# Kernel optimization log

Hardware: AMD Instinct MI355X
Metric: run time of the kernel (lower is better)

Reference implementation:

```python
import jax, jax.numpy as jnp
import numpy as np

B, P, ENC, DEC, ATT, EMB, V, MEM, TCAP = 64, 196, 2048, 512, 512, 512, 10000, 128, 22
T = TCAP - 1  # max decode length (caption_lengths - 1)


def setup_inputs() -> dict:
    key = jax.random.key(0)
    ks = iter(jax.random.split(key, 32))
    def w(shape, s=0.02):
        return (jax.random.normal(next(ks), shape, jnp.float32) * s)
    encoder_out = jax.random.normal(next(ks), (B, P, ENC), jnp.float32)
    encoded_captions = jax.random.randint(next(ks), (B, TCAP), 0, V)
    lens = np.sort(np.asarray(jax.random.randint(next(ks), (B,), 5, TCAP + 1)))[::-1].copy()
    lens[0] = TCAP  # ensure max(decode_lengths) == T
    caption_lengths = jnp.asarray(lens, jnp.int32)
    return {
        'encoder_out': encoder_out,
        'encoded_captions': encoded_captions,
        'caption_lengths': caption_lengths,
        'emb_table': w((V, EMB), 0.05),
        # Linear weights stored as [in, out] (torch W.T), so y = x @ W + b
        'W_enc': w((ENC, ATT)), 'b_enc': jnp.zeros((ATT,), jnp.float32),
        'W_dec': w((DEC, ATT)), 'b_dec': jnp.zeros((ATT,), jnp.float32),
        'W_full': w((ATT, 1)), 'b_full': jnp.zeros((1,), jnp.float32),
        'W_inith': w((ENC, DEC)), 'b_inith': jnp.zeros((DEC,), jnp.float32),
        'W_initc': w((ENC, DEC)), 'b_initc': jnp.zeros((DEC,), jnp.float32),
        'W_beta': w((DEC, ENC)), 'b_beta': jnp.zeros((ENC,), jnp.float32),
        # LSTMCell (torch gate order i, f, g, o), stored as [in, 4*dec]
        'W_ih': w((EMB + ENC, 4 * DEC)), 'b_ih': jnp.zeros((4 * DEC,), jnp.float32),
        'W_hh': w((DEC, 4 * DEC)), 'b_hh': jnp.zeros((4 * DEC,), jnp.float32),
        'memory_bank': jax.random.normal(next(ks), (MEM, DEC), jnp.float32),
        'W_fc': w((DEC, V)), 'b_fc': jnp.zeros((V,), jnp.float32),
    }


def _decode(encoder_out, encoded_captions, caption_lengths, emb_table,
            W_enc, b_enc, W_dec, b_dec, W_full, b_full,
            W_inith, b_inith, W_initc, b_initc, W_beta, b_beta,
            W_ih, b_ih, W_hh, b_hh, memory_bank, W_fc, b_fc):
    dec_len = caption_lengths - 1  # decode_lengths
    embs = emb_table[encoded_captions]                 # [B, TCAP, EMB]
    mean_enc = encoder_out.mean(axis=1)                # [B, ENC]
    h0 = mean_enc @ W_inith + b_inith
    c0 = mean_enc @ W_initc + b_initc
    att1 = encoder_out @ W_enc + b_enc                 # [B, P, ATT] precomputed

    x_seq = jnp.swapaxes(embs[:, :T, :], 0, 1)         # [T, B, EMB]
    mask_seq = jnp.arange(T)[:, None] < dec_len[None, :]  # [T, B]

    def step(carry, inp):
        h, c = carry
        x_t, m = inp                                   # [B,EMB], [B]
        # attention
        att2 = h @ W_dec + b_dec                       # [B, ATT]
        e = (jax.nn.relu(att1 + att2[:, None, :]) @ W_full)[..., 0] + b_full[0]  # [B, P]
        alpha = jax.nn.softmax(e, axis=1)
        awe = jnp.einsum('bpe,bp->be', encoder_out, alpha)  # [B, ENC]
        gate = jax.nn.sigmoid(h @ W_beta + b_beta)
        awe = gate * awe
        # LSTMCell
        xi = jnp.concatenate([x_t, awe], axis=1)
        gates = xi @ W_ih + b_ih + h @ W_hh + b_hh      # [B, 4*DEC]
        gi, gf, gg, go = jnp.split(gates, 4, axis=1)
        c_new = jax.nn.sigmoid(gf) * c + jax.nn.sigmoid(gi) * jnp.tanh(gg)
        h_new = jax.nn.sigmoid(go) * jnp.tanh(c_new)
        # hash memory
        sim = h_new @ memory_bank.T                    # [B, MEM]
        h_new = h_new + jax.nn.softmax(sim, axis=1) @ memory_bank
        # fc (dropout = identity in eval)
        preds = h_new @ W_fc + b_fc                    # [B, V]
        m2 = m[:, None]
        h = jnp.where(m2, h_new, h)
        c = jnp.where(m2, c_new, c)
        preds = jnp.where(m2, preds, 0.0)
        alpha = jnp.where(m2, alpha, 0.0)
        return (h, c), (preds, alpha)

    (_, _), (preds_seq, alpha_seq) = jax.lax.scan(step, (h0, c0), (x_seq, mask_seq))
    predictions = jnp.swapaxes(preds_seq, 0, 1)        # [B, T, V]
    alphas = jnp.swapaxes(alpha_seq, 0, 1)             # [B, T, P]
    return predictions, dec_len, alphas


def reference(encoder_out, encoded_captions, caption_lengths, emb_table,
              W_enc, b_enc, W_dec, b_dec, W_full, b_full,
              W_inith, b_inith, W_initc, b_initc, W_beta, b_beta,
              W_ih, b_ih, W_hh, b_hh, memory_bank, W_fc, b_fc):
    return _decode(encoder_out, encoded_captions, caption_lengths, emb_table,
                   W_enc, b_enc, W_dec, b_dec, W_full, b_full,
                   W_inith, b_inith, W_initc, b_initc, W_beta, b_beta,
                   W_ih, b_ih, W_hh, b_hh, memory_bank, W_fc, b_fc)
```

## Files before the change

kernel.cpp:

```cpp
#include <hip/hip_runtime.h>

#define BB   64
#define PP   196
#define ENCD 2048
#define DECD 512
#define VV   10000
#define TT   21
#define KIH  2560

typedef __attribute__((ext_vector_type(8))) short bf16x8;
typedef __attribute__((ext_vector_type(4))) float f32x4;

__device__ __forceinline__ float sigm(float x)   { return 1.f / (1.f + __expf(-x)); }
__device__ __forceinline__ float tanh_f(float x) { return 1.f - 2.f / (1.f + __expf(2.f * x)); }
__device__ __forceinline__ ushort f2bf(float x) {
    unsigned u = __float_as_uint(x);
    unsigned r = (u + 0x7FFFu + ((u >> 16) & 1u)) >> 16;
    return (ushort)r;
}
__device__ __forceinline__ float bf2f(short u) {
    return __uint_as_float(((unsigned)(ushort)u) << 16);
}
union U8 { float4 f4; ushort u[8]; };


__global__ void k_cvt(const float* __restrict__ in, ushort* __restrict__ out, int n4) {
    int i = blockIdx.x * 256 + threadIdx.x;
    if (i >= n4) return;
    float4 v = ((const float4*)in)[i];
    ushort4 o; o.x = f2bf(v.x); o.y = f2bf(v.y); o.z = f2bf(v.z); o.w = f2bf(v.w);
    ((ushort4*)out)[i] = o;
}

__global__ void k_mean16(const ushort* __restrict__ encB, float* __restrict__ mean) {
    int idx = blockIdx.x * 256 + threadIdx.x;
    int b = idx >> 10, e2 = idx & 1023;
    const uint* p = (const uint*)encB + (size_t)b * PP * 1024 + e2;
    float s0 = 0.f, s1 = 0.f;
    #pragma unroll 7
    for (int i = 0; i < PP; ++i) {
        uint v = p[(size_t)i * 1024];
        s0 += __uint_as_float(v << 16);
        s1 += __uint_as_float(v & 0xffff0000u);
    }
    mean[b * 2048 + e2 * 2]     = s0 * (1.f / 196.f);
    mean[b * 2048 + e2 * 2 + 1] = s1 * (1.f / 196.f);
}

__global__ __launch_bounds__(256) void k_ipart(const float* __restrict__ mean,
        const float* __restrict__ Wh, const float* __restrict__ Wc,
        float* __restrict__ ipart) {
    __shared__ alignas(16) float As[32][68];
    __shared__ alignas(16) float Bs[32][68];
    const int n0 = blockIdx.x * 64;
    const int kc = blockIdx.y;
    const int mat = blockIdx.z;
    const float* Bp = mat ? Wc : Wh;
    const int tid = threadIdx.x, tx = tid & 15, ty = tid >> 4;
    float acc[4][4] = {};
    for (int k0 = 0; k0 < 512; k0 += 32) {
        #pragma unroll
        for (int p = 0; p < 2; ++p) {
            int c = p * 256 + tid;
            int m = c >> 3, k4 = (c & 7) * 4;
            float4 v = *(const float4*)(mean + m * 2048 + kc * 512 + k0 + k4);
            As[k4 + 0][m] = v.x; As[k4 + 1][m] = v.y; As[k4 + 2][m] = v.z; As[k4 + 3][m] = v.w;
            int kb = c >> 4, n4 = (c & 15) * 4;
            float4 w = *(const float4*)(Bp + (size_t)(kc * 512 + k0 + kb) * 512 + n0 + n4);
            *(float4*)&Bs[kb][n4] = w;
        }
        __syncthreads();
        #pragma unroll 8
        for (int k = 0; k < 32; ++k) {
            float4 a = *(const float4*)&As[k][ty * 4];
            float4 b = *(const float4*)&Bs[k][tx * 4];
            float av[4] = {a.x, a.y, a.z, a.w}, bv[4] = {b.x, b.y, b.z, b.w};
            #pragma unroll
            for (int i = 0; i < 4; ++i)
                #pragma unroll
                for (int j = 0; j < 4; ++j) acc[i][j] += av[i] * bv[j];
        }
        __syncthreads();
    }
    #pragma unroll
    for (int i = 0; i < 4; ++i) {
        int m = ty * 4 + i;
        #pragma unroll
        for (int j = 0; j < 4; ++j) {
            int n = n0 + tx * 4 + j;
            ipart[((size_t)(mat * 4 + kc) * BB + m) * 512 + n] = acc[i][j];
        }
    }
}

__global__ void k_ifin(const float* __restrict__ ipart,
                       const float* __restrict__ bh, const float* __restrict__ bc,
                       float* __restrict__ h, float* __restrict__ c, ushort* __restrict__ hB) {
    int idx = blockIdx.x * 256 + threadIdx.x;
    int mat = idx >> 15, rem = idx & 32767;
    int b = rem >> 9, d = rem & 511;
    float s = 0.f;
    #pragma unroll
    for (int kc = 0; kc < 4; ++kc) s += ipart[((size_t)(mat * 4 + kc) * BB + b) * 512 + d];
    if (mat) c[rem] = s + bc[d];
    else { float v = s + bh[d]; h[rem] = v; hB[rem] = f2bf(v); }
}

__global__ __launch_bounds__(256) void k_tcvt_all(
        const float* __restrict__ Wenc, const float* __restrict__ Wdec,
        const float* __restrict__ Wbeta, const float* __restrict__ Whh,
        const float* __restrict__ Wih, const float* __restrict__ Wfc,
        ushort* __restrict__ WencT, ushort* __restrict__ WdecT,
        ushort* __restrict__ WbetaT, ushort* __restrict__ WhhT,
        ushort* __restrict__ WihT, ushort* __restrict__ WfcT) {
    __shared__ float lds[64 * 65];
    int l = blockIdx.x;
    const float* in; ushort* out; int K, N, KT;
    if (l < 256)       { in = Wenc;  out = WencT;  K = 2048; N = 512;   KT = 32; }
    else if (l < 320)  { l -= 256;  in = Wdec;  out = WdecT;  K = 512;  N = 512;   KT = 8; }
    else if (l < 576)  { l -= 320;  in = Wbeta; out = WbetaT; K = 512;  N = 2048;  KT = 8; }
    else if (l < 832)  { l -= 576;  in = Whh;   out = WhhT;   K = 512;  N = 2048;  KT = 8; }
    else if (l < 2112) { l -= 832;  in = Wih;   out = WihT;   K = KIH;  N = 2048;  KT = 40; }
    else               { l -= 2112; in = Wfc;   out = WfcT;   K = 512;  N = 10000; KT = 8; }
    const int k0 = (l % KT) * 64, n0 = (l / KT) * 64;
    const int tid = threadIdx.x;
    for (int i = tid; i < 4096; i += 256) {
        int kk = i >> 6, nn = i & 63;
        float v = 0.f;
        if (n0 + nn < N) v = in[(size_t)(k0 + kk) * N + n0 + nn];
        lds[nn * 65 + kk] = v;
    }
    __syncthreads();
    for (int i = tid; i < 4096; i += 256) {
        int nn = i >> 6, kk = i & 63;
        out[(size_t)(n0 + nn) * K + k0 + kk] = f2bf(lds[nn * 65 + kk]);
    }
}

__global__ __launch_bounds__(256) void k_att1_256(const ushort* __restrict__ A,
        const ushort* __restrict__ Bt, const float* __restrict__ bias,
        ushort* __restrict__ C) {
    __shared__ alignas(16) ushort As[64 * 64];
    __shared__ alignas(16) ushort Bs[256 * 64];
    const int n0 = blockIdx.x * 256;
    const int m0 = blockIdx.y * 64;
    const int tid = threadIdx.x, wid = tid >> 6, lane = tid & 63;
    f32x4 acc[4][4] = {};
    for (int k0 = 0; k0 < 2048; k0 += 64) {
        #pragma unroll
        for (int p = 0; p < 2; ++p) {
            int c = p * 256 + tid;
            int r = c >> 3, cc = c & 7;
            float4 v = *(const float4*)(A + (size_t)(m0 + r) * 2048 + k0 + cc * 8);
            *(float4*)(As + r * 64 + ((cc ^ (r & 7)) * 8)) = v;
        }
        #pragma unroll
        for (int p = 0; p < 8; ++p) {
            int c = p * 256 + tid;
            int r = c >> 3, cc = c & 7;
            float4 v = *(const float4*)(Bt + (size_t)(n0 + r) * 2048 + k0 + cc * 8);
            *(float4*)(Bs + r * 64 + ((cc ^ (r & 7)) * 8)) = v;
        }
        __syncthreads();
        #pragma unroll
        for (int kk = 0; kk < 2; ++kk) {
            int ci = kk * 4 + (lane >> 4);
            bf16x8 afrag[4], bfrag[4];
            #pragma unroll
            for (int m = 0; m < 4; ++m) {
                int row = m * 16 + (lane & 15);
                afrag[m] = *(const bf16x8*)(As + row * 64 + ((ci ^ (row & 7)) * 8));
            }
            #pragma unroll
            for (int n = 0; n < 4; ++n) {
                int col = wid * 64 + n * 16 + (lane & 15);
                bfrag[n] = *(const bf16x8*)(Bs + col * 64 + ((ci ^ (col & 7)) * 8));
            }
            #pragma unroll
            for (int m = 0; m < 4; ++m)
                #pragma unroll
                for (int n = 0; n < 4; ++n)
                    acc[m][n] = __builtin_amdgcn_mfma_f32_16x16x32_bf16(afrag[m], bfrag[n], acc[m][n], 0, 0, 0);
        }
        __syncthreads();
    }
    #pragma unroll
    for (int m = 0; m < 4; ++m) {
        int rb = m0 + m * 16 + (lane >> 4) * 4;
        #pragma unroll
        for (int n = 0; n < 4; ++n) {
            int col = n0 + wid * 64 + n * 16 + (lane & 15);
            float bv = bias[col];
            #pragma unroll
            for (int r = 0; r < 4; ++r)
                C[(size_t)(rb + r) * 512 + col] = f2bf(acc[m][n][r] + bv);
        }
    }
}

__global__ void k_declen(const int* __restrict__ lens, float* __restrict__ out) {
    int b = threadIdx.x;
    if (b < BB) out[b] = (float)(lens[b] - 1);
}


__global__ __launch_bounds__(256) void k_hgemm64(const ushort* __restrict__ hB,
        const float* __restrict__ emb, const int* __restrict__ caps, int t,
        const ushort* __restrict__ WdecT, const float* __restrict__ bd,
        const ushort* __restrict__ WbetaT, const float* __restrict__ bb,
        const ushort* __restrict__ WhhT, const ushort* __restrict__ WihT,
        float* __restrict__ att2, float* __restrict__ gate, float* __restrict__ hhp) {
    __shared__ alignas(16) ushort As[64 * 64];
    __shared__ alignas(16) ushort Bs[64 * 64];
    __shared__ int capsh[64];
    const int bx = blockIdx.x;
    int seg, n0;
    if (bx < 8)       { seg = 0; n0 = bx * 64; }
    else if (bx < 40) { seg = 1; n0 = (bx - 8) * 64; }
    else              { seg = 2; n0 = (bx - 40) * 64; }
    const int tid = threadIdx.x, wid = tid >> 6, lane = tid & 63;
    if (tid < 64) capsh[tid] = caps[tid * 22 + t];
    __syncthreads();
    const int KSEG = (seg == 2) ? 1024 : 512;
    f32x4 acc[4] = {};
    for (int k0 = 0; k0 < KSEG; k0 += 64) {
        const bool second = k0 >= 512;
        #pragma unroll
        for (int p = 0; p < 2; ++p) {
            int c = p * 256 + tid;
            int r = c >> 3, cc = c & 7;
            if (!second) {
                float4 v = *(const float4*)(hB + r * 512 + k0 + cc * 8);
                *(float4*)(As + r * 64 + ((cc ^ (r & 7)) * 8)) = v;
            } else {
                const float* er = emb + (size_t)capsh[r] * 512 + (k0 - 512) + cc * 8;
                float4 v0 = *(const float4*)er;
                float4 v1 = *(const float4*)(er + 4);
                U8 pk;
                pk.u[0] = f2bf(v0.x); pk.u[1] = f2bf(v0.y); pk.u[2] = f2bf(v0.z); pk.u[3] = f2bf(v0.w);
                pk.u[4] = f2bf(v1.x); pk.u[5] = f2bf(v1.y); pk.u[6] = f2bf(v1.z); pk.u[7] = f2bf(v1.w);
                *(float4*)(As + r * 64 + ((cc ^ (r & 7)) * 8)) = pk.f4;
            }
            const ushort* brow;
            if (seg == 0)      brow = WdecT + (size_t)(n0 + r) * 512 + k0 + cc * 8;
            else if (seg == 1) brow = WbetaT + (size_t)(n0 + r) * 512 + k0 + cc * 8;
            else brow = second ? (WihT + (size_t)(n0 + r) * KIH + (k0 - 512) + cc * 8)
                               : (WhhT + (size_t)(n0 + r) * 512 + k0 + cc * 8);
            float4 v = *(const float4*)brow;
            *(float4*)(Bs + r * 64 + ((cc ^ (r & 7)) * 8)) = v;
        }
        __syncthreads();
        #pragma unroll
        for (int kk = 0; kk < 2; ++kk) {
            int ci = kk * 4 + (lane >> 4);
            int colL = wid * 16 + (lane & 15);
            bf16x8 bfrag = *(const bf16x8*)(Bs + colL * 64 + ((ci ^ (colL & 7)) * 8));
            #pragma unroll
            for (int m = 0; m < 4; ++m) {
                int row = m * 16 + (lane & 15);
                bf16x8 afrag = *(const bf16x8*)(As + row * 64 + ((ci ^ (row & 7)) * 8));
                acc[m] = __builtin_amdgcn_mfma_f32_16x16x32_bf16(afrag, bfrag, acc[m], 0, 0, 0);
            }
        }
        __syncthreads();
    }
    int colL = wid * 16 + (lane & 15);
    int col = n0 + colL;
    #pragma unroll
    for (int m = 0; m < 4; ++m) {
        int rb = m * 16 + (lane >> 4) * 4;
        #pragma unroll
        for (int r = 0; r < 4; ++r) {
            int row = rb + r;
            float v = acc[m][r];
            if (seg == 0)      att2[row * 512 + col] = v + bd[col];
            else if (seg == 1) gate[row * 2048 + col] = sigm(v + bb[col]);
            else               hhp[(size_t)row * 2048 + col] = v;
        }
    }
}

__global__ __launch_bounds__(256) void k_escore_p(const ushort* __restrict__ att1B,
        const float* __restrict__ att2, const float* __restrict__ Wf,
        float* __restrict__ es) {
    __shared__ float a2[512], wf[512];
    int b = blockIdx.y, pc = blockIdx.x, tid = threadIdx.x;
    for (int i = tid; i < 512; i += 256) { a2[i] = att2[b * 512 + i]; wf[i] = Wf[i]; }
    __syncthreads();
    int lane = tid & 63, wid = tid >> 6;
    for (int i = wid; i < 49; i += 4) {
        int p = pc * 49 + i;
        bf16x8 rv = *(const bf16x8*)(att1B + ((size_t)(b * PP + p)) * 512 + lane * 8);
        float s = 0.f;
        #pragma unroll
        for (int j = 0; j < 8; ++j) {
            float v = bf2f(rv[j]) + a2[lane * 8 + j];
            s += (v > 0.f ? v : 0.f) * wf[lane * 8 + j];
        }
        #pragma unroll
        for (int off = 32; off; off >>= 1) s += __shfl_down(s, off);
        if (lane == 0) es[b * 256 + p] = s;
    }
}

__global__ __launch_bounds__(256) void k_awe16s(const ushort* __restrict__ encB,
        const float* __restrict__ es, const float* __restrict__ gate,
        const int* __restrict__ lens, int t,
        uint* __restrict__ aweB, float* __restrict__ out_alpha) {
    __shared__ float al[224], red[256];
    int b = blockIdx.y, pc = blockIdx.x, tid = threadIdx.x;
    float v = (tid < PP) ? es[b * 256 + tid] : -3.4e38f;
    red[tid] = v; __syncthreads();
    for (int s = 128; s; s >>= 1) { if (tid < s) red[tid] = fmaxf(red[tid], red[tid + s]); __syncthreads(); }
    float mx = red[0]; __syncthreads();
    float ev = (tid < PP) ? __expf(v - mx) : 0.f;
    red[tid] = ev; __syncthreads();
    for (int s = 128; s; s >>= 1) { if (tid < s) red[tid] += red[tid + s]; __syncthreads(); }
    float inv = 1.f / red[0];
    if (tid < PP) {
        float a = ev * inv;
        al[tid] = a;
        if (pc == 0) {
            bool m = t < (lens[b] - 1);
            out_alpha[((size_t)b * TT + t) * PP + tid] = m ? a : 0.f;
        }
    }
    __syncthreads();
    int pair = pc * 128 + (tid >> 1);
    int half = tid & 1;
    const uint* p = (const uint*)encB + (size_t)b * PP * 1024 + pair;
    float s0 = 0.f, s1 = 0.f;
    int i0 = half * 98;
    #pragma unroll 7
    for (int i = i0; i < i0 + 98; ++i) {
        uint vv = p[(size_t)i * 1024];
        float a = al[i];
        s0 += a * __uint_as_float(vv << 16);
        s1 += a * __uint_as_float(vv & 0xffff0000u);
    }
    s0 += __shfl_xor(s0, 1);
    s1 += __shfl_xor(s1, 1);
    if (half == 0) {
        int e = pair * 2;
        float g0 = s0 * gate[b * 2048 + e];
        float g1 = s1 * gate[b * 2048 + e + 1];
        aweB[b * 1024 + pair] = (uint)f2bf(g0) | ((uint)f2bf(g1) << 16);
    }
}

__global__ __launch_bounds__(256) void k_gawe64(const ushort* __restrict__ aweB,
        const ushort* __restrict__ WihT, float* __restrict__ pawe) {
    __shared__ alignas(16) ushort As[64 * 64];
    __shared__ alignas(16) ushort Bs[64 * 64];
    const int n0 = blockIdx.x * 64;
    const int kc = blockIdx.y;
    const int tid = threadIdx.x, wid = tid >> 6, lane = tid & 63;
    f32x4 acc[4] = {};
    for (int k0 = 0; k0 < 512; k0 += 64) {
        #pragma unroll
        for (int p = 0; p < 2; ++p) {
            int c = p * 256 + tid;
            int r = c >> 3, cc = c & 7;
            float4 v = *(const float4*)(aweB + r * 2048 + kc * 512 + k0 + cc * 8);
            *(float4*)(As + r * 64 + ((cc ^ (r & 7)) * 8)) = v;
            float4 w = *(const float4*)(WihT + (size_t)(n0 + r) * KIH + 512 + kc * 512 + k0 + cc * 8);
            *(float4*)(Bs + r * 64 + ((cc ^ (r & 7)) * 8)) = w;
        }
        __syncthreads();
        #pragma unroll
        for (int kk = 0; kk < 2; ++kk) {
            int ci = kk * 4 + (lane >> 4);
            int colL = wid * 16 + (lane & 15);
            bf16x8 bfrag = *(const bf16x8*)(Bs + colL * 64 + ((ci ^ (colL & 7)) * 8));
            #pragma unroll
            for (int m = 0; m < 4; ++m) {
                int row = m * 16 + (lane & 15);
                bf16x8 afrag = *(const bf16x8*)(As + row * 64 + ((ci ^ (row & 7)) * 8));
                acc[m] = __builtin_amdgcn_mfma_f32_16x16x32_bf16(afrag, bfrag, acc[m], 0, 0, 0);
            }
        }
        __syncthreads();
    }
    int col = n0 + wid * 16 + (lane & 15);
    #pragma unroll
    for (int m = 0; m < 4; ++m) {
        int rb = m * 16 + (lane >> 4) * 4;
        #pragma unroll
        for (int r = 0; r < 4; ++r)
            pawe[((size_t)kc * BB + rb + r) * 2048 + col] = acc[m][r];
    }
}

__global__ __launch_bounds__(256) void k_memattn(const float* __restrict__ hhp,
        const float* __restrict__ pawe,
        const float* __restrict__ bih, const float* __restrict__ bhh,
        const int* __restrict__ lens, int t, const float* __restrict__ memB,
        float* __restrict__ h, float* __restrict__ c,
        ushort* __restrict__ hB, ushort* __restrict__ histB) {
    __shared__ float hs[512], sims[128], red[256], ps[128];
    int b = blockIdx.x, tid = threadIdx.x;
    bool msk = t < (lens[b] - 1);
    for (int j = tid; j < 512; j += 256) {
        float g[4];
        #pragma unroll
        for (int q = 0; q < 4; ++q) {
            int col = q * 512 + j;
            float s = bih[col] + bhh[col] + hhp[(size_t)b * 2048 + col];
            #pragma unroll
            for (int kc = 0; kc < 4; ++kc) s += pawe[((size_t)kc * BB + b) * 2048 + col];
            g[q] = s;
        }
        float gi = sigm(g[0]), gf = sigm(g[1]), gg = tanh_f(g[2]), go = sigm(g[3]);
        float cold = c[b * 512 + j];
        float cn = gf * cold + gi * gg;
        c[b * 512 + j] = msk ? cn : cold;
        hs[j] = go * tanh_f(cn);
    }
    __syncthreads();
    int lane = tid & 63, wid = tid >> 6;
    for (int m = wid * 32; m < wid * 32 + 32; ++m) {
        const float* r = memB + (size_t)m * 512 + lane * 8;
        float4 r0 = *(const float4*)(r);
        float4 r1 = *(const float4*)(r + 4);
        float4 h0 = *(const float4*)(&hs[lane * 8]);
        float4 h1 = *(const float4*)(&hs[lane * 8 + 4]);
        float s = r0.x * h0.x + r0.y * h0.y + r0.z * h0.z + r0.w * h0.w
                + r1.x * h1.x + r1.y * h1.y + r1.z * h1.z + r1.w * h1.w;
        #pragma unroll
        for (int off = 32; off; off >>= 1) s += __shfl_down(s, off);
        if (lane == 0) sims[m] = s;
    }
    __syncthreads();
    float v = (tid < 128) ? sims[tid] : -3.4e38f;
    red[tid] = v; __syncthreads();
    for (int s = 128; s; s >>= 1) { if (tid < s) red[tid] = fmaxf(red[tid], red[tid + s]); __syncthreads(); }
    float mx = red[0]; __syncthreads();
    float ev = (tid < 128) ? __expf(v - mx) : 0.f;
    red[tid] = ev; __syncthreads();
    for (int s = 128; s; s >>= 1) { if (tid < s) red[tid] += red[tid + s]; __syncthreads(); }
    if (tid < 128) ps[tid] = ev / red[0];
    __syncthreads();
    for (int d = tid; d < 512; d += 256) {
        float s = 0.f;
        #pragma unroll 4
        for (int m = 0; m < 128; ++m) s += ps[m] * memB[(size_t)m * 512 + d];
        float hn = hs[d] + s;
        histB[((size_t)t * BB + b) * 512 + d] = f2bf(hn);
        float hold = h[b * 512 + d];
        float hv = msk ? hn : hold;
        h[b * 512 + d] = hv;
        hB[b * 512 + d] = f2bf(hv);
    }
}

__global__ __launch_bounds__(256) void k_preds_batch(const ushort* __restrict__ histB,
        const ushort* __restrict__ WfcT, const float* __restrict__ bfc,
        const int* __restrict__ lens, float* __restrict__ out) {
    __shared__ alignas(16) ushort As[64 * 64];
    __shared__ alignas(16) ushort Bs[256 * 64];
    const int n0 = blockIdx.x * 256;
    const int t = blockIdx.y;
    const ushort* A = histB + (size_t)t * BB * 512;
    const int tid = threadIdx.x, wid = tid >> 6, lane = tid & 63;
    f32x4 acc[4][4] = {};
    for (int k0 = 0; k0 < 512; k0 += 64) {
        #pragma unroll
        for (int p = 0; p < 2; ++p) {
            int c = p * 256 + tid;
            int r = c >> 3, cc = c & 7;
            float4 v = *(const float4*)(A + r * 512 + k0 + cc * 8);
            *(float4*)(As + r * 64 + ((cc ^ (r & 7)) * 8)) = v;
        }
        #pragma unroll
        for (int p = 0; p < 8; ++p) {
            int c = p * 256 + tid;
            int r = c >> 3, cc = c & 7;
            float4 v = *(const float4*)(WfcT + (size_t)(n0 + r) * 512 + k0 + cc * 8);
            *(float4*)(Bs + r * 64 + ((cc ^ (r & 7)) * 8)) = v;
        }
        __syncthreads();
        #pragma unroll
        for (int kk = 0; kk < 2; ++kk) {
            int ci = kk * 4 + (lane >> 4);
            bf16x8 afrag[4], bfrag[4];
            #pragma unroll
            for (int m = 0; m < 4; ++m) {
                int row = m * 16 + (lane & 15);
                afrag[m] = *(const bf16x8*)(As + row * 64 + ((ci ^ (row & 7)) * 8));
            }
            #pragma unroll
            for (int n = 0; n < 4; ++n) {
                int col = wid * 64 + n * 16 + (lane & 15);
                bfrag[n] = *(const bf16x8*)(Bs + col * 64 + ((ci ^ (col & 7)) * 8));
            }
            #pragma unroll
            for (int m = 0; m < 4; ++m)
                #pragma unroll
                for (int n = 0; n < 4; ++n)
                    acc[m][n] = __builtin_amdgcn_mfma_f32_16x16x32_bf16(afrag[m], bfrag[n], acc[m][n], 0, 0, 0);
        }
        __syncthreads();
    }
    #pragma unroll
    for (int m = 0; m < 4; ++m) {
        int rb = m * 16 + (lane >> 4) * 4;
        #pragma unroll
        for (int n = 0; n < 4; ++n) {
            int col = n0 + wid * 64 + n * 16 + (lane & 15);
            if (col < VV) {
                float bv = bfc[col];
                #pragma unroll
                for (int r = 0; r < 4; ++r) {
                    int b = rb + r;
                    bool msk = t < (lens[b] - 1);
                    out[((size_t)b * TT + t) * VV + col] = msk ? (acc[m][n][r] + bv) : 0.f;
                }
            }
        }
    }
}


extern "C" void kernel_launch(void* const* d_in, const int* in_sizes, int n_in,
                              void* d_out, int out_size, void* d_ws, size_t ws_size,
                              hipStream_t stream) {
    const float* enc     = (const float*)d_in[0];
    const int*   caps    = (const int*)d_in[1];
    const int*   lens    = (const int*)d_in[2];
    const float* emb     = (const float*)d_in[3];
    const float* W_enc   = (const float*)d_in[4];
    const float* b_enc   = (const float*)d_in[5];
    const float* W_dec   = (const float*)d_in[6];
    const float* b_dec   = (const float*)d_in[7];
    const float* W_full  = (const float*)d_in[8];
    const float* W_inith = (const float*)d_in[10];
    const float* b_inith = (const float*)d_in[11];
    const float* W_initc = (const float*)d_in[12];
    const float* b_initc = (const float*)d_in[13];
    const float* W_beta  = (const float*)d_in[14];
    const float* b_beta  = (const float*)d_in[15];
    const float* W_ih    = (const float*)d_in[16];
    const float* b_ih    = (const float*)d_in[17];
    const float* W_hh    = (const float*)d_in[18];
    const float* b_hh    = (const float*)d_in[19];
    const float* memB    = (const float*)d_in[20];
    const float* W_fc    = (const float*)d_in[21];
    const float* b_fc    = (const float*)d_in[22];

    float* out = (float*)d_out;
    float* preds_out  = out;
    float* declen_out = out + (size_t)BB * TT * VV;
    float* alpha_out  = declen_out + BB;

    float* ws    = (float*)d_ws;
    ushort* att1B = (ushort*)ws;        ws += (size_t)12544 * 512 / 2;
    float* h     = ws;  ws += BB * DECD;
    float* c     = ws;  ws += BB * DECD;
    float* att2  = ws;  ws += BB * 512;
    float* gate  = ws;  ws += BB * ENCD;
    float* es    = ws;  ws += BB * 256;
    float* hhp   = ws;  ws += BB * 2048;
    float* pawe  = ws;  ws += (size_t)4 * BB * 2048;
    ushort* hB   = (ushort*)ws;  ws += BB * DECD / 2;
    uint*  aweB  = (uint*)ws;    ws += BB * ENCD / 2;
    ushort* histB = (ushort*)ws; ws += (size_t)TT * BB * DECD / 2;
    ushort* encB  = (ushort*)ws; ws += (size_t)12544 * 2048 / 2;
    ushort* WencT = (ushort*)ws; ws += (size_t)512 * 2048 / 2;
    ushort* WfcT  = (ushort*)ws; ws += (size_t)10240 * 512 / 2;
    ushort* WdecT = (ushort*)ws; ws += (size_t)512 * 512 / 2;
    ushort* WbetaT= (ushort*)ws; ws += (size_t)2048 * 512 / 2;
    ushort* WhhT  = (ushort*)ws; ws += (size_t)2048 * 512 / 2;
    ushort* WihT  = (ushort*)ws; ws += (size_t)2048 * KIH / 2;
    float* ipart = hhp;
    float* mean  = (float*)att1B;

    k_cvt<<<(12544 * 2048 / 4 + 255) / 256, 256, 0, stream>>>(enc, encB, 12544 * 2048 / 4);
    k_mean16<<<256, 256, 0, stream>>>(encB, mean);
    k_ipart<<<dim3(8, 4, 2), 256, 0, stream>>>(mean, W_inith, W_initc, ipart);
    k_ifin<<<256, 256, 0, stream>>>(ipart, b_inith, b_initc, h, c, hB);
    k_declen<<<1, 64, 0, stream>>>(lens, declen_out);
    k_tcvt_all<<<3392, 256, 0, stream>>>(W_enc, W_dec, W_beta, W_hh, W_ih, W_fc,
                                         WencT, WdecT, WbetaT, WhhT, WihT, WfcT);
    k_att1_256<<<dim3(2, 196), 256, 0, stream>>>(encB, WencT, b_enc, att1B);

    for (int t = 0; t < TT; ++t) {
        k_hgemm64<<<72, 256, 0, stream>>>(hB, emb, caps, t, WdecT, b_dec, WbetaT, b_beta,
                                          WhhT, WihT, att2, gate, hhp);
        k_escore_p<<<dim3(4, 64), 256, 0, stream>>>(att1B, att2, W_full, es);
        k_awe16s<<<dim3(8, 64), 256, 0, stream>>>(encB, es, gate, lens, t, aweB, alpha_out);
        k_gawe64<<<dim3(32, 4), 256, 0, stream>>>((const ushort*)aweB, WihT, pawe);
        k_memattn<<<64, 256, 0, stream>>>(hhp, pawe, b_ih, b_hh, lens, t, memB, h, c, hB, histB);
    }
    k_preds_batch<<<dim3(40, TT), 256, 0, stream>>>(histB, WfcT, b_fc, lens, preds_out);
}
```

Measured before the change: 1.965 ms.

## Fuse per-step decode into one persistent per-batch kernel with fp16 dot2 weights

Replaces the five per-timestep kernel launches with a single persistent kernel that uses one 1024-thread block per batch row. Each block keeps h, c, gates and attention state in shared memory and loops over all timesteps internally. The embedding part of the LSTM input projection is precomputed for all timesteps with one MFMA GEMM. The recurrent weights are repacked as fp16 pairs and consumed with packed dot2 instructions instead of bf16 MFMA tiles. This removes launch overhead and global round-trips between stages. In exchange, every block re-streams the full weight matrices from cache at each step, only 64 blocks run on the device, and weight precision changes from bf16 to fp16.

```diff
diff --git a/kernel.cpp b/kernel.cpp
--- a/kernel.cpp
+++ b/kernel.cpp
@@ -6,10 +6,10 @@
 #define DECD 512
 #define VV   10000
 #define TT   21
-#define KIH  2560
 
 typedef __attribute__((ext_vector_type(8))) short bf16x8;
 typedef __attribute__((ext_vector_type(4))) float f32x4;
+typedef __fp16 f16x2 __attribute__((ext_vector_type(2)));
 
 __device__ __forceinline__ float sigm(float x)   { return 1.f / (1.f + __expf(-x)); }
 __device__ __forceinline__ float tanh_f(float x) { return 1.f - 2.f / (1.f + __expf(2.f * x)); }
@@ -18,10 +18,21 @@
     unsigned r = (u + 0x7FFFu + ((u >> 16) & 1u)) >> 16;
     return (ushort)r;
 }
-__device__ __forceinline__ float bf2f(short u) {
-    return __uint_as_float(((unsigned)(ushort)u) << 16);
-}
-union U8 { float4 f4; ushort u[8]; };
+__device__ __forceinline__ float bf2f(ushort u) {
+    return __uint_as_float(((unsigned)u) << 16);
+}
+__device__ __forceinline__ uint pk2(float a, float b) {
+    f16x2 p = __builtin_amdgcn_cvt_pkrtz(a, b);
+    return *(uint*)&p;
+}
+__device__ __forceinline__ float dot2(uint w, uint x, float c) {
+#if __has_builtin(__builtin_amdgcn_fdot2)
+    return __builtin_amdgcn_fdot2(*(f16x2*)&w, *(f16x2*)&x, c, false);
+#else
+    f16x2 a = *(f16x2*)&w, b = *(f16x2*)&x;
+    return c + (float)a[0] * (float)b[0] + (float)a[1] * (float)b[1];
+#endif
+}
 
 
 __global__ void k_cvt(const float* __restrict__ in, ushort* __restrict__ out, int n4) {
@@ -95,33 +106,28 @@
 
 __global__ void k_ifin(const float* __restrict__ ipart,
                        const float* __restrict__ bh, const float* __restrict__ bc,
-                       float* __restrict__ h, float* __restrict__ c, ushort* __restrict__ hB) {
+                       float* __restrict__ h0, float* __restrict__ c0) {
     int idx = blockIdx.x * 256 + threadIdx.x;
     int mat = idx >> 15, rem = idx & 32767;
     int b = rem >> 9, d = rem & 511;
     float s = 0.f;
     #pragma unroll
     for (int kc = 0; kc < 4; ++kc) s += ipart[((size_t)(mat * 4 + kc) * BB + b) * 512 + d];
-    if (mat) c[rem] = s + bc[d];
-    else { float v = s + bh[d]; h[rem] = v; hB[rem] = f2bf(v); }
+    if (mat) c0[rem] = s + bc[d];
+    else     h0[rem] = s + bh[d];
 }
 
 __global__ __launch_bounds__(256) void k_tcvt_all(
-        const float* __restrict__ Wenc, const float* __restrict__ Wdec,
-        const float* __restrict__ Wbeta, const float* __restrict__ Whh,
-        const float* __restrict__ Wih, const float* __restrict__ Wfc,
-        ushort* __restrict__ WencT, ushort* __restrict__ WdecT,
-        ushort* __restrict__ WbetaT, ushort* __restrict__ WhhT,
-        ushort* __restrict__ WihT, ushort* __restrict__ WfcT) {
+        const float* __restrict__ Wenc, const float* __restrict__ Wih,
+        const float* __restrict__ Wfc,
+        ushort* __restrict__ WencT, ushort* __restrict__ WihT0,
+        ushort* __restrict__ WfcT) {
     __shared__ float lds[64 * 65];
     int l = blockIdx.x;
     const float* in; ushort* out; int K, N, KT;
-    if (l < 256)       { in = Wenc;  out = WencT;  K = 2048; N = 512;   KT = 32; }
-    else if (l < 320)  { l -= 256;  in = Wdec;  out = WdecT;  K = 512;  N = 512;   KT = 8; }
-    else if (l < 576)  { l -= 320;  in = Wbeta; out = WbetaT; K = 512;  N = 2048;  KT = 8; }
-    else if (l < 832)  { l -= 576;  in = Whh;   out = WhhT;   K = 512;  N = 2048;  KT = 8; }
-    else if (l < 2112) { l -= 832;  in = Wih;   out = WihT;   K = KIH;  N = 2048;  KT = 40; }
-    else               { l -= 2112; in = Wfc;   out = WfcT;   K = 512;  N = 10000; KT = 8; }
+    if (l < 256)      { in = Wenc; out = WencT; K = 2048; N = 512;   KT = 32; }
+    else if (l < 512) { l -= 256; in = Wih;  out = WihT0; K = 512; N = 2048;  KT = 8; }
+    else              { l -= 512; in = Wfc;  out = WfcT;  K = 512; N = 10000; KT = 8; }
     const int k0 = (l % KT) * 64, n0 = (l / KT) * 64;
     const int tid = threadIdx.x;
     for (int i = tid; i < 4096; i += 256) {
@@ -137,7 +143,26 @@
     }
 }
 
-__global__ __launch_bounds__(256) void k_att1_256(const ushort* __restrict__ A,
+__global__ void k_packcat(const float* __restrict__ Wd, const float* __restrict__ Wb,
+                          const float* __restrict__ Wh, uint* __restrict__ out) {
+    int idx = blockIdx.x * 256 + threadIdx.x;
+    int k2 = idx / 5120, n = idx % 5120;
+    int k = k2 * 2;
+    float a = 0.f, b2 = 0.f;
+    if (n < 512)       { a = Wd[(size_t)k * 512 + n];           b2 = Wd[(size_t)(k + 1) * 512 + n]; }
+    else if (n < 2560) { int nn = n - 512;  a = Wb[(size_t)k * 2048 + nn]; b2 = Wb[(size_t)(k + 1) * 2048 + nn]; }
+    else if (n < 4608) { int nn = n - 2560; a = Wh[(size_t)k * 2048 + nn]; b2 = Wh[(size_t)(k + 1) * 2048 + nn]; }
+    out[idx] = pk2(a, b2);
+}
+
+__global__ void k_packih(const float* __restrict__ Wih, uint* __restrict__ out) {
+    int idx = blockIdx.x * 256 + threadIdx.x;
+    int k2 = idx >> 11, n = idx & 2047;
+    int r0 = 512 + k2 * 2;
+    out[idx] = pk2(Wih[(size_t)r0 * 2048 + n], Wih[(size_t)(r0 + 1) * 2048 + n]);
+}
+
+__global__ __launch_bounds__(256) void k_att1n(const ushort* __restrict__ A,
         const ushort* __restrict__ Bt, const float* __restrict__ bias,
         ushort* __restrict__ C) {
     __shared__ alignas(16) ushort As[64 * 64];
@@ -198,258 +223,242 @@
     }
 }
 
+__global__ __launch_bounds__(256) void k_xpre(const float* __restrict__ emb,
+        const int* __restrict__ caps, const ushort* __restrict__ WihT0,
+        float* __restrict__ xpre) {
+    __shared__ alignas(16) ushort As[64 * 64];
+    __shared__ alignas(16) ushort Bs[256 * 64];
+    __shared__ int capsh[64];
+    const int n0 = blockIdx.x * 256;
+    const int t = blockIdx.y;
+    const int tid = threadIdx.x, wid = tid >> 6, lane = tid & 63;
+    if (tid < 64) capsh[tid] = caps[tid * 22 + t];
+    __syncthreads();
+    f32x4 acc[4][4] = {};
+    for (int k0 = 0; k0 < 512; k0 += 64) {
+        #pragma unroll
+        for (int p = 0; p < 2; ++p) {
+            int c = p * 256 + tid;
+            int r = c >> 3, cc = c & 7;
+            const float* er = emb + (size_t)capsh[r] * 512 + k0 + cc * 8;
+            float4 v0 = *(const float4*)er;
+            float4 v1 = *(const float4*)(er + 4);
+            union { float4 f4; ushort u[8]; } pk;
+            pk.u[0] = f2bf(v0.x); pk.u[1] = f2bf(v0.y); pk.u[2] = f2bf(v0.z); pk.u[3] = f2bf(v0.w);
+            pk.u[4] = f2bf(v1.x); pk.u[5] = f2bf(v1.y); pk.u[6] = f2bf(v1.z); pk.u[7] = f2bf(v1.w);
+            *(float4*)(As + r * 64 + ((cc ^ (r & 7)) * 8)) = pk.f4;
+        }
+        #pragma unroll
+        for (int p = 0; p < 8; ++p) {
+            int c = p * 256 + tid;
+            int r = c >> 3, cc = c & 7;
+            float4 v = *(const float4*)(WihT0 + (size_t)(n0 + r) * 512 + k0 + cc * 8);
+            *(float4*)(Bs + r * 64 + ((cc ^ (r & 7)) * 8)) = v;
+        }
+        __syncthreads();
+        #pragma unroll
+        for (int kk = 0; kk < 2; ++kk) {
+            int ci = kk * 4 + (lane >> 4);
+            bf16x8 afrag[4], bfrag[4];
+            #pragma unroll
+            for (int m = 0; m < 4; ++m) {
+                int row = m * 16 + (lane & 15);
+                afrag[m] = *(const bf16x8*)(As + row * 64 + ((ci ^ (row & 7)) * 8));
+            }
+            #pragma unroll
+            for (int n = 0; n < 4; ++n) {
+                int col = wid * 64 + n * 16 + (lane & 15);
+                bfrag[n] = *(const bf16x8*)(Bs + col * 64 + ((ci ^ (col & 7)) * 8));
+            }
+            #pragma unroll
+            for (int m = 0; m < 4; ++m)
+                #pragma unroll
+                for (int n = 0; n < 4; ++n)
+                    acc[m][n] = __builtin_amdgcn_mfma_f32_16x16x32_bf16(afrag[m], bfrag[n], acc[m][n], 0, 0, 0);
+        }
+        __syncthreads();
+    }
+    #pragma unroll
+    for (int m = 0; m < 4; ++m) {
+        int rb = m * 16 + (lane >> 4) * 4;
+        #pragma unroll
+        for (int n = 0; n < 4; ++n) {
+            int col = n0 + wid * 64 + n * 16 + (lane & 15);
+            #pragma unroll
+            for (int r = 0; r < 4; ++r)
+                xpre[((size_t)t * BB + rb + r) * 2048 + col] = acc[m][n][r];
+        }
+    }
+}
+
 __global__ void k_declen(const int* __restrict__ lens, float* __restrict__ out) {
     int b = threadIdx.x;
     if (b < BB) out[b] = (float)(lens[b] - 1);
 }
 
 
-__global__ __launch_bounds__(256) void k_hgemm64(const ushort* __restrict__ hB,
-        const float* __restrict__ emb, const int* __restrict__ caps, int t,
-        const ushort* __restrict__ WdecT, const float* __restrict__ bd,
-        const ushort* __restrict__ WbetaT, const float* __restrict__ bb,
-        const ushort* __restrict__ WhhT, const ushort* __restrict__ WihT,
-        float* __restrict__ att2, float* __restrict__ gate, float* __restrict__ hhp) {
-    __shared__ alignas(16) ushort As[64 * 64];
-    __shared__ alignas(16) ushort Bs[64 * 64];
-    __shared__ int capsh[64];
-    const int bx = blockIdx.x;
-    int seg, n0;
-    if (bx < 8)       { seg = 0; n0 = bx * 64; }
-    else if (bx < 40) { seg = 1; n0 = (bx - 8) * 64; }
-    else              { seg = 2; n0 = (bx - 40) * 64; }
-    const int tid = threadIdx.x, wid = tid >> 6, lane = tid & 63;
-    if (tid < 64) capsh[tid] = caps[tid * 22 + t];
+struct MArgs {
+    const int* lens; const float* h0; const float* c0;
+    const uint* WcatPK; const float* bd; const float* bb;
+    const ushort* att1B; const float* Wf; const uint* encU;
+    const uint* WihPK; const float* xpre;
+    const float* bih; const float* bhh; const float* memB;
+    ushort* histB; float* alpha_out;
+};
+
+__global__ __launch_bounds__(1024) void k_mega(MArgs a) {
+    __shared__ uint hpk[256];
+    __shared__ float att2F[512];
+    __shared__ float gateF[2048];
+    __shared__ float hhpF[2048];
+    __shared__ float xg[2048];
+    __shared__ uint awepk[1024];
+    __shared__ float cF[512], hF[512];
+    __shared__ float esS[200], alphaS[200], wfS[512], red[256], simsS[128], psS[128];
+    const int b = blockIdx.x, tid = threadIdx.x;
+    const int lenb = a.lens[b];
+
+    if (tid < 512) {
+        hF[tid]  = a.h0[b * 512 + tid];
+        cF[tid]  = a.c0[b * 512 + tid];
+        wfS[tid] = a.Wf[tid];
+    }
     __syncthreads();
-    const int KSEG = (seg == 2) ? 1024 : 512;
-    f32x4 acc[4] = {};
-    for (int k0 = 0; k0 < KSEG; k0 += 64) {
-        const bool second = k0 >= 512;
-        #pragma unroll
-        for (int p = 0; p < 2; ++p) {
-            int c = p * 256 + tid;
-            int r = c >> 3, cc = c & 7;
-            if (!second) {
-                float4 v = *(const float4*)(hB + r * 512 + k0 + cc * 8);
-                *(float4*)(As + r * 64 + ((cc ^ (r & 7)) * 8)) = v;
-            } else {
-                const float* er = emb + (size_t)capsh[r] * 512 + (k0 - 512) + cc * 8;
-                float4 v0 = *(const float4*)er;
-                float4 v1 = *(const float4*)(er + 4);
-                U8 pk;
-                pk.u[0] = f2bf(v0.x); pk.u[1] = f2bf(v0.y); pk.u[2] = f2bf(v0.z); pk.u[3] = f2bf(v0.w);
-                pk.u[4] = f2bf(v1.x); pk.u[5] = f2bf(v1.y); pk.u[6] = f2bf(v1.z); pk.u[7] = f2bf(v1.w);
-                *(float4*)(As + r * 64 + ((cc ^ (r & 7)) * 8)) = pk.f4;
-            }
-            const ushort* brow;
-            if (seg == 0)      brow = WdecT + (size_t)(n0 + r) * 512 + k0 + cc * 8;
-            else if (seg == 1) brow = WbetaT + (size_t)(n0 + r) * 512 + k0 + cc * 8;
-            else brow = second ? (WihT + (size_t)(n0 + r) * KIH + (k0 - 512) + cc * 8)
-                               : (WhhT + (size_t)(n0 + r) * 512 + k0 + cc * 8);
-            float4 v = *(const float4*)brow;
-            *(float4*)(Bs + r * 64 + ((cc ^ (r & 7)) * 8)) = v;
-        }
-        __syncthreads();
-        #pragma unroll
-        for (int kk = 0; kk < 2; ++kk) {
-            int ci = kk * 4 + (lane >> 4);
-            int colL = wid * 16 + (lane & 15);
-            bf16x8 bfrag = *(const bf16x8*)(Bs + colL * 64 + ((ci ^ (colL & 7)) * 8));
-            #pragma unroll
-            for (int m = 0; m < 4; ++m) {
-                int row = m * 16 + (lane & 15);
-                bf16x8 afrag = *(const bf16x8*)(As + row * 64 + ((ci ^ (row & 7)) * 8));
-                acc[m] = __builtin_amdgcn_mfma_f32_16x16x32_bf16(afrag, bfrag, acc[m], 0, 0, 0);
-            }
-        }
-        __syncthreads();
-    }
-    int colL = wid * 16 + (lane & 15);
-    int col = n0 + colL;
-    #pragma unroll
-    for (int m = 0; m < 4; ++m) {
-        int rb = m * 16 + (lane >> 4) * 4;
-        #pragma unroll
-        for (int r = 0; r < 4; ++r) {
-            int row = rb + r;
-            float v = acc[m][r];
-            if (seg == 0)      att2[row * 512 + col] = v + bd[col];
-            else if (seg == 1) gate[row * 2048 + col] = sigm(v + bb[col]);
-            else               hhp[(size_t)row * 2048 + col] = v;
-        }
-    }
-}
-
-__global__ __launch_bounds__(256) void k_escore_p(const ushort* __restrict__ att1B,
-        const float* __restrict__ att2, const float* __restrict__ Wf,
-        float* __restrict__ es) {
-    __shared__ float a2[512], wf[512];
-    int b = blockIdx.y, pc = blockIdx.x, tid = threadIdx.x;
-    for (int i = tid; i < 512; i += 256) { a2[i] = att2[b * 512 + i]; wf[i] = Wf[i]; }
+    if (tid < 256) hpk[tid] = pk2(hF[2 * tid], hF[2 * tid + 1]);
     __syncthreads();
-    int lane = tid & 63, wid = tid >> 6;
-    for (int i = wid; i < 49; i += 4) {
-        int p = pc * 49 + i;
-        bf16x8 rv = *(const bf16x8*)(att1B + ((size_t)(b * PP + p)) * 512 + lane * 8);
-        float s = 0.f;
-        #pragma unroll
-        for (int j = 0; j < 8; ++j) {
-            float v = bf2f(rv[j]) + a2[lane * 8 + j];
-            s += (v > 0.f ? v : 0.f) * wf[lane * 8 + j];
-        }
-        #pragma unroll
-        for (int off = 32; off; off >>= 1) s += __shfl_down(s, off);
-        if (lane == 0) es[b * 256 + p] = s;
-    }
-}
-
-__global__ __launch_bounds__(256) void k_awe16s(const ushort* __restrict__ encB,
-        const float* __restrict__ es, const float* __restrict__ gate,
-        const int* __restrict__ lens, int t,
-        uint* __restrict__ aweB, float* __restrict__ out_alpha) {
-    __shared__ float al[224], red[256];
-    int b = blockIdx.y, pc = blockIdx.x, tid = threadIdx.x;
-    float v = (tid < PP) ? es[b * 256 + tid] : -3.4e38f;
-    red[tid] = v; __syncthreads();
-    for (int s = 128; s; s >>= 1) { if (tid < s) red[tid] = fmaxf(red[tid], red[tid + s]); __syncthreads(); }
-    float mx = red[0]; __syncthreads();
-    float ev = (tid < PP) ? __expf(v - mx) : 0.f;
-    red[tid] = ev; __syncthreads();
-    for (int s = 128; s; s >>= 1) { if (tid < s) red[tid] += red[tid + s]; __syncthreads(); }
-    float inv = 1.f / red[0];
-    if (tid < PP) {
-        float a = ev * inv;
-        al[tid] = a;
-        if (pc == 0) {
-            bool m = t < (lens[b] - 1);
-            out_alpha[((size_t)b * TT + t) * PP + tid] = m ? a : 0.f;
-        }
-    }
-    __syncthreads();
-    int pair = pc * 128 + (tid >> 1);
-    int half = tid & 1;
-    const uint* p = (const uint*)encB + (size_t)b * PP * 1024 + pair;
-    float s0 = 0.f, s1 = 0.f;
-    int i0 = half * 98;
-    #pragma unroll 7
-    for (int i = i0; i < i0 + 98; ++i) {
-        uint vv = p[(size_t)i * 1024];
-        float a = al[i];
-        s0 += a * __uint_as_float(vv << 16);
-        s1 += a * __uint_as_float(vv & 0xffff0000u);
-    }
-    s0 += __shfl_xor(s0, 1);
-    s1 += __shfl_xor(s1, 1);
-    if (half == 0) {
-        int e = pair * 2;
-        float g0 = s0 * gate[b * 2048 + e];
-        float g1 = s1 * gate[b * 2048 + e + 1];
-        aweB[b * 1024 + pair] = (uint)f2bf(g0) | ((uint)f2bf(g1) << 16);
-    }
-}
-
-__global__ __launch_bounds__(256) void k_gawe64(const ushort* __restrict__ aweB,
-        const ushort* __restrict__ WihT, float* __restrict__ pawe) {
-    __shared__ alignas(16) ushort As[64 * 64];
-    __shared__ alignas(16) ushort Bs[64 * 64];
-    const int n0 = blockIdx.x * 64;
-    const int kc = blockIdx.y;
-    const int tid = threadIdx.x, wid = tid >> 6, lane = tid & 63;
-    f32x4 acc[4] = {};
-    for (int k0 = 0; k0 < 512; k0 += 64) {
-        #pragma unroll
-        for (int p = 0; p < 2; ++p) {
-            int c = p * 256 + tid;
-            int r = c >> 3, cc = c & 7;
-            float4 v = *(const float4*)(aweB + r * 2048 + kc * 512 + k0 + cc * 8);
-            *(float4*)(As + r * 64 + ((cc ^ (r & 7)) * 8)) = v;
-            float4 w = *(const float4*)(WihT + (size_t)(n0 + r) * KIH + 512 + kc * 512 + k0 + cc * 8);
-            *(float4*)(Bs + r * 64 + ((cc ^ (r & 7)) * 8)) = w;
-        }
-        __syncthreads();
-        #pragma unroll
-        for (int kk = 0; kk < 2; ++kk) {
-            int ci = kk * 4 + (lane >> 4);
-            int colL = wid * 16 + (lane & 15);
-            bf16x8 bfrag = *(const bf16x8*)(Bs + colL * 64 + ((ci ^ (colL & 7)) * 8));
-            #pragma unroll
-            for (int m = 0; m < 4; ++m) {
-                int row = m * 16 + (lane & 15);
-                bf16x8 afrag = *(const bf16x8*)(As + row * 64 + ((ci ^ (row & 7)) * 8));
-                acc[m] = __builtin_amdgcn_mfma_f32_16x16x32_bf16(afrag, bfrag, acc[m], 0, 0, 0);
-            }
-        }
-        __syncthreads();
-    }
-    int col = n0 + wid * 16 + (lane & 15);
-    #pragma unroll
-    for (int m = 0; m < 4; ++m) {
-        int rb = m * 16 + (lane >> 4) * 4;
-        #pragma unroll
-        for (int r = 0; r < 4; ++r)
-            pawe[((size_t)kc * BB + rb + r) * 2048 + col] = acc[m][r];
-    }
-}
-
-__global__ __launch_bounds__(256) void k_memattn(const float* __restrict__ hhp,
-        const float* __restrict__ pawe,
-        const float* __restrict__ bih, const float* __restrict__ bhh,
-        const int* __restrict__ lens, int t, const float* __restrict__ memB,
-        float* __restrict__ h, float* __restrict__ c,
-        ushort* __restrict__ hB, ushort* __restrict__ histB) {
-    __shared__ float hs[512], sims[128], red[256], ps[128];
-    int b = blockIdx.x, tid = threadIdx.x;
-    bool msk = t < (lens[b] - 1);
-    for (int j = tid; j < 512; j += 256) {
-        float g[4];
-        #pragma unroll
-        for (int q = 0; q < 4; ++q) {
-            int col = q * 512 + j;
-            float s = bih[col] + bhh[col] + hhp[(size_t)b * 2048 + col];
-            #pragma unroll
-            for (int kc = 0; kc < 4; ++kc) s += pawe[((size_t)kc * BB + b) * 2048 + col];
-            g[q] = s;
-        }
-        float gi = sigm(g[0]), gf = sigm(g[1]), gg = tanh_f(g[2]), go = sigm(g[3]);
-        float cold = c[b * 512 + j];
-        float cn = gf * cold + gi * gg;
-        c[b * 512 + j] = msk ? cn : cold;
-        hs[j] = go * tanh_f(cn);
-    }
-    __syncthreads();
-    int lane = tid & 63, wid = tid >> 6;
-    for (int m = wid * 32; m < wid * 32 + 32; ++m) {
-        const float* r = memB + (size_t)m * 512 + lane * 8;
-        float4 r0 = *(const float4*)(r);
-        float4 r1 = *(const float4*)(r + 4);
-        float4 h0 = *(const float4*)(&hs[lane * 8]);
-        float4 h1 = *(const float4*)(&hs[lane * 8 + 4]);
-        float s = r0.x * h0.x + r0.y * h0.y + r0.z * h0.z + r0.w * h0.w
-                + r1.x * h1.x + r1.y * h1.y + r1.z * h1.z + r1.w * h1.w;
-        #pragma unroll
-        for (int off = 32; off; off >>= 1) s += __shfl_down(s, off);
-        if (lane == 0) sims[m] = s;
-    }
-    __syncthreads();
-    float v = (tid < 128) ? sims[tid] : -3.4e38f;
-    red[tid] = v; __syncthreads();
-    for (int s = 128; s; s >>= 1) { if (tid < s) red[tid] = fmaxf(red[tid], red[tid + s]); __syncthreads(); }
-    float mx = red[0]; __syncthreads();
-    float ev = (tid < 128) ? __expf(v - mx) : 0.f;
-    red[tid] = ev; __syncthreads();
-    for (int s = 128; s; s >>= 1) { if (tid < s) red[tid] += red[tid + s]; __syncthreads(); }
-    if (tid < 128) ps[tid] = ev / red[0];
-    __syncthreads();
-    for (int d = tid; d < 512; d += 256) {
-        float s = 0.f;
-        #pragma unroll 4
-        for (int m = 0; m < 128; ++m) s += ps[m] * memB[(size_t)m * 512 + d];
-        float hn = hs[d] + s;
-        histB[((size_t)t * BB + b) * 512 + d] = f2bf(hn);
-        float hold = h[b * 512 + d];
-        float hv = msk ? hn : hold;
-        h[b * 512 + d] = hv;
-        hB[b * 512 + d] = f2bf(hv);
+
+    for (int t = 0; t < TT; ++t) {
+        const bool msk = t < lenb - 1;
+        {
+            float a0 = 0.f, a1 = 0.f, a2 = 0.f, a3 = 0.f, a4 = 0.f;
+            #pragma unroll 4
+            for (int k2 = 0; k2 < 256; ++k2) {
+                uint xp = hpk[k2];
+                const uint* wr = a.WcatPK + (size_t)k2 * 5120 + tid;
+                a0 = dot2(wr[0],    xp, a0);
+                a1 = dot2(wr[1024], xp, a1);
+                a2 = dot2(wr[2048], xp, a2);
+                a3 = dot2(wr[3072], xp, a3);
+                a4 = dot2(wr[4096], xp, a4);
+            }
+            float av[5] = {a0, a1, a2, a3, a4};
+            #pragma unroll
+            for (int i = 0; i < 5; ++i) {
+                int n = tid + i * 1024;
+                if (n < 512)        att2F[n] = av[i] + a.bd[n];
+                else if (n < 2560)  gateF[n - 512] = sigm(av[i] + a.bb[n - 512]);
+                else if (n < 4608)  hhpF[n - 2560] = av[i];
+            }
+        }
+        __syncthreads();
+        if (tid < 784) {
+            int p = tid >> 2, q = tid & 3;
+            const ushort* row = a.att1B + ((size_t)(b * PP + p)) * 512 + q * 128;
+            float e = 0.f;
+            for (int kk = 0; kk < 16; ++kk) {
+                bf16x8 rv = *(const bf16x8*)(row + kk * 8);
+                int kb = q * 128 + kk * 8;
+                #pragma unroll
+                for (int j = 0; j < 8; ++j) {
+                    float v = bf2f((ushort)rv[j]) + att2F[kb + j];
+                    e += (v > 0.f ? v : 0.f) * wfS[kb + j];
+                }
+            }
+            e += __shfl_xor(e, 1); e += __shfl_xor(e, 2);
+            if (q == 0) esS[p] = e;
+        }
+        __syncthreads();
+        if (tid < 256) red[tid] = (tid < PP) ? esS[tid] : -3.4e38f;
+        __syncthreads();
+        for (int s = 128; s; s >>= 1) { if (tid < s) red[tid] = fmaxf(red[tid], red[tid + s]); __syncthreads(); }
+        float smx = red[0];
+        __syncthreads();
+        float sev = 0.f;
+        if (tid < 256) { sev = (tid < PP) ? __expf(esS[tid] - smx) : 0.f; red[tid] = sev; }
+        __syncthreads();
+        for (int s = 128; s; s >>= 1) { if (tid < s) red[tid] += red[tid + s]; __syncthreads(); }
+        float sinv = 1.f / red[0];
+        if (tid < PP) {
+            float al = sev * sinv;
+            alphaS[tid] = al;
+            a.alpha_out[((size_t)b * TT + t) * PP + tid] = msk ? al : 0.f;
+        }
+        __syncthreads();
+        {
+            const uint* pp = a.encU + ((size_t)b * PP) * 1024 + tid;
+            float s0 = 0.f, s1 = 0.f;
+            #pragma unroll 7
+            for (int p = 0; p < PP; ++p) {
+                uint vv = pp[(size_t)p * 1024];
+                float al = alphaS[p];
+                s0 += al * __uint_as_float(vv << 16);
+                s1 += al * __uint_as_float(vv & 0xffff0000u);
+            }
+            float g0 = s0 * gateF[2 * tid], g1 = s1 * gateF[2 * tid + 1];
+            awepk[tid] = pk2(g0, g1);
+        }
+        __syncthreads();
+        {
+            float g0 = 0.f, g1 = 0.f;
+            #pragma unroll 4
+            for (int k2 = 0; k2 < 1024; ++k2) {
+                uint xp = awepk[k2];
+                const uint* wr = a.WihPK + (size_t)k2 * 2048 + tid;
+                g0 = dot2(wr[0],    xp, g0);
+                g1 = dot2(wr[1024], xp, g1);
+            }
+            const float* xp = a.xpre + ((size_t)t * BB + b) * 2048;
+            int n0 = tid, n1 = tid + 1024;
+            xg[n0] = g0 + a.bih[n0] + a.bhh[n0] + hhpF[n0] + xp[n0];
+            xg[n1] = g1 + a.bih[n1] + a.bhh[n1] + hhpF[n1] + xp[n1];
+        }
+        __syncthreads();
+        if (tid < 512) {
+            int d = tid;
+            float gi = sigm(xg[d]), gf = sigm(xg[512 + d]);
+            float gg = tanh_f(xg[1024 + d]), go = sigm(xg[1536 + d]);
+            float cn = gf * cF[d] + gi * gg;
+            cF[d] = msk ? cn : cF[d];
+            att2F[d] = go * tanh_f(cn);
+        }
+        __syncthreads();
+        {
+            int mm = tid >> 3, q = tid & 7;
+            const float* r = a.memB + (size_t)mm * 512 + q * 64;
+            const float* hsp = att2F + q * 64;
+            float s = 0.f;
+            #pragma unroll
+            for (int d = 0; d < 64; d += 4) {
+                float4 rv = *(const float4*)(r + d);
+                s += rv.x * hsp[d] + rv.y * hsp[d + 1] + rv.z * hsp[d + 2] + rv.w * hsp[d + 3];
+            }
+            s += __shfl_xor(s, 1); s += __shfl_xor(s, 2); s += __shfl_xor(s, 4);
+            if (q == 0) simsS[mm] = s;
+        }
+        __syncthreads();
+        if (tid < 256) red[tid] = (tid < 128) ? simsS[tid] : -3.4e38f;
+        __syncthreads();
+        for (int s = 128; s; s >>= 1) { if (tid < s) red[tid] = fmaxf(red[tid], red[tid + s]); __syncthreads(); }
+        float mmx = red[0];
+        __syncthreads();
+        float mev = 0.f;
+        if (tid < 256) { mev = (tid < 128) ? __expf(simsS[tid] - mmx) : 0.f; red[tid] = mev; }
+        __syncthreads();
+        for (int s = 128; s; s >>= 1) { if (tid < s) red[tid] += red[tid + s]; __syncthreads(); }
+        if (tid < 128) psS[tid] = mev / red[0];
+        __syncthreads();
+        if (tid < 512) {
+            int d = tid;
+            float s = 0.f;
+            #pragma unroll 4
+            for (int m = 0; m < 128; ++m) s += psS[m] * a.memB[(size_t)m * 512 + d];
+            float hn = att2F[d] + s;
+            a.histB[((size_t)t * BB + b) * 512 + d] = f2bf(hn);
+            hF[d] = msk ? hn : hF[d];
+        }
+        __syncthreads();
+        if (tid < 256) hpk[tid] = pk2(hF[2 * tid], hF[2 * tid + 1]);
+        __syncthreads();
     }
 }
 
@@ -553,43 +562,39 @@
     float* alpha_out  = declen_out + BB;
 
     float* ws    = (float*)d_ws;
-    ushort* att1B = (ushort*)ws;        ws += (size_t)12544 * 512 / 2;
-    float* h     = ws;  ws += BB * DECD;
-    float* c     = ws;  ws += BB * DECD;
-    float* att2  = ws;  ws += BB * 512;
-    float* gate  = ws;  ws += BB * ENCD;
-    float* es    = ws;  ws += BB * 256;
-    float* hhp   = ws;  ws += BB * 2048;
-    float* pawe  = ws;  ws += (size_t)4 * BB * 2048;
-    ushort* hB   = (ushort*)ws;  ws += BB * DECD / 2;
-    uint*  aweB  = (uint*)ws;    ws += BB * ENCD / 2;
+    ushort* att1B = (ushort*)ws;  ws += (size_t)12544 * 512 / 2;
+    float* h0    = ws;  ws += BB * DECD;
+    float* c0    = ws;  ws += BB * DECD;
+    float* xpre  = ws;  ws += (size_t)TT * BB * 2048;
     ushort* histB = (ushort*)ws; ws += (size_t)TT * BB * DECD / 2;
     ushort* encB  = (ushort*)ws; ws += (size_t)12544 * 2048 / 2;
     ushort* WencT = (ushort*)ws; ws += (size_t)512 * 2048 / 2;
     ushort* WfcT  = (ushort*)ws; ws += (size_t)10240 * 512 / 2;
-    ushort* WdecT = (ushort*)ws; ws += (size_t)512 * 512 / 2;
-    ushort* WbetaT= (ushort*)ws; ws += (size_t)2048 * 512 / 2;
-    ushort* WhhT  = (ushort*)ws; ws += (size_t)2048 * 512 / 2;
-    ushort* WihT  = (ushort*)ws; ws += (size_t)2048 * KIH / 2;
-    float* ipart = hhp;
+    ushort* WihT0 = (ushort*)ws; ws += (size_t)2048 * 512 / 2;
+    uint*  WcatPK = (uint*)ws;   ws += (size_t)256 * 5120;
+    uint*  WihPK  = (uint*)ws;   ws += (size_t)1024 * 2048;
     float* mean  = (float*)att1B;
+    float* ipart = xpre;
 
     k_cvt<<<(12544 * 2048 / 4 + 255) / 256, 256, 0, stream>>>(enc, encB, 12544 * 2048 / 4);
     k_mean16<<<256, 256, 0, stream>>>(encB, mean);
     k_ipart<<<dim3(8, 4, 2), 256, 0, stream>>>(mean, W_inith, W_initc, ipart);
-    k_ifin<<<256, 256, 0, stream>>>(ipart, b_inith, b_initc, h, c, hB);
+    k_ifin<<<256, 256, 0, stream>>>(ipart, b_inith, b_initc, h0, c0);
     k_declen<<<1, 64, 0, stream>>>(lens, declen_out);
-    k_tcvt_all<<<3392, 256, 0, stream>>>(W_enc, W_dec, W_beta, W_hh, W_ih, W_fc,
-                                         WencT, WdecT, WbetaT, WhhT, WihT, WfcT);
-    k_att1_256<<<dim3(2, 196), 256, 0, stream>>>(encB, WencT, b_enc, att1B);
-
-    for (int t = 0; t < TT; ++t) {
-        k_hgemm64<<<72, 256, 0, stream>>>(hB, emb, caps, t, WdecT, b_dec, WbetaT, b_beta,
-                                          WhhT, WihT, att2, gate, hhp);
-        k_escore_p<<<dim3(4, 64), 256, 0, stream>>>(att1B, att2, W_full, es);
-        k_awe16s<<<dim3(8, 64), 256, 0, stream>>>(encB, es, gate, lens, t, aweB, alpha_out);
-        k_gawe64<<<dim3(32, 4), 256, 0, stream>>>((const ushort*)aweB, WihT, pawe);
-        k_memattn<<<64, 256, 0, stream>>>(hhp, pawe, b_ih, b_hh, lens, t, memB, h, c, hB, histB);
-    }
+    k_tcvt_all<<<1768, 256, 0, stream>>>(W_enc, W_ih, W_fc, WencT, WihT0, WfcT);
+    k_att1n<<<dim3(2, 196), 256, 0, stream>>>(encB, WencT, b_enc, att1B);
+    k_xpre<<<dim3(8, TT), 256, 0, stream>>>(emb, caps, WihT0, xpre);
+    k_packcat<<<(256 * 5120) / 256, 256, 0, stream>>>(W_dec, W_beta, W_hh, WcatPK);
+    k_packih<<<(1024 * 2048) / 256, 256, 0, stream>>>(W_ih, WihPK);
+
+    MArgs ma;
+    ma.lens = lens; ma.h0 = h0; ma.c0 = c0;
+    ma.WcatPK = WcatPK; ma.bd = b_dec; ma.bb = b_beta;
+    ma.att1B = att1B; ma.Wf = W_full; ma.encU = (const uint*)encB;
+    ma.WihPK = WihPK; ma.xpre = xpre;
+    ma.bih = b_ih; ma.bhh = b_hh; ma.memB = memB;
+    ma.histB = histB; ma.alpha_out = alpha_out;
+    k_mega<<<BB, 1024, 0, stream>>>(ma);
+
     k_preds_batch<<<dim3(40, TT), 256, 0, stream>>>(histB, WfcT, b_fc, lens, preds_out);
 }
```

Result: slower. 4.213 ms (+114.4%).
